# Performance work log

Measured on AMD Instinct MI355X. Metric: run time of the kernel, lower is better.

Reference implementation:

```python
import jax, jax.numpy as jnp
import numpy as np

N = 10000      # nodes
E = 160000     # edges
F_IN = 84
H = 256
P = 4          # powers [0,1,2,3]
L = 3          # mixhop layers


def setup_inputs() -> dict:
    key = jax.random.key(0)
    ks = jax.random.split(key, 10)
    s = 0.05
    inp = {}
    inp["x"] = jax.random.normal(ks[0], (N, F_IN), jnp.float32)
    inp["edge_index"] = jax.random.randint(ks[1], (2, E), 0, N, dtype=jnp.int32)
    inp["w_in"] = jax.random.normal(ks[2], (F_IN, H), jnp.float32) * s
    inp["b_in"] = jnp.zeros((H,), jnp.float32)
    inp["mh_w0"] = jax.random.normal(ks[3], (P, H, H), jnp.float32) * s
    inp["mh_b0"] = jnp.zeros((P, H), jnp.float32)
    inp["mh_w12"] = jax.random.normal(ks[4], (2, P, P * H, H), jnp.float32) * s
    inp["mh_b12"] = jnp.zeros((2, P, H), jnp.float32)
    inp["ln_g"] = jnp.ones((L, P * H), jnp.float32)
    inp["ln_b"] = jnp.zeros((L, P * H), jnp.float32)
    inp["w1"] = jax.random.normal(ks[5], (P * H, H), jnp.float32) * s
    inp["b1"] = jnp.zeros((H,), jnp.float32)
    inp["w2"] = jax.random.normal(ks[6], (H, H // 2), jnp.float32) * s
    inp["b2"] = jnp.zeros((H // 2,), jnp.float32)
    inp["w3"] = jax.random.normal(ks[7], (H // 2, 1), jnp.float32) * s
    inp["b3"] = jnp.zeros((1,), jnp.float32)
    return inp


def _gcn_norm(edge_index, n):
    # D^{-1/2} (A + I) D^{-1/2}, PyG gcn_norm with add_self_loops=True
    loop = jnp.arange(n, dtype=edge_index.dtype)
    src = jnp.concatenate([edge_index[0], loop])
    dst = jnp.concatenate([edge_index[1], loop])
    deg = jax.ops.segment_sum(jnp.ones(src.shape[0], jnp.float32), dst, num_segments=n)
    dinv = jnp.where(deg > 0, deg ** -0.5, 0.0)
    return src, dst, dinv[src] * dinv[dst]


def _propagate(h, src, dst, w, n):
    # out[i] = sum_{(j->i)} w_e * h[j]
    return jax.ops.segment_sum(h[src] * w[:, None], dst, num_segments=n)


def _mixhop(h, src, dst, w, n, W, B):
    outs = [h @ W[0] + B[0]]  # power 0
    for p in range(1, W.shape[0]):
        h = _propagate(h, src, dst, w, n)
        outs.append(h @ W[p] + B[p])
    return jnp.concatenate(outs, axis=-1)  # [n, P*H]


def _layernorm(x, g, b, eps=1e-5):
    mu = x.mean(-1, keepdims=True)
    var = x.var(-1, keepdims=True)
    return (x - mu) * jax.lax.rsqrt(var + eps) * g + b


def reference(x, edge_index, w_in, b_in, mh_w0, mh_b0, mh_w12, mh_b12,
              ln_g, ln_b, w1, b1, w2, b2, w3, b3):
    gelu = lambda t: jax.nn.gelu(t, approximate=False)  # torch default (erf)
    n = x.shape[0]
    src, dst, w = _gcn_norm(edge_index, n)
    h = gelu(x @ w_in + b_in)
    for i in range(L):
        W, B = (mh_w0, mh_b0) if i == 0 else (mh_w12[i - 1], mh_b12[i - 1])
        h = _mixhop(h, src, dst, w, n, W, B)
        h = gelu(_layernorm(h, ln_g[i], ln_b[i]))
        # dropout inactive at inference
    h = gelu(h @ w1 + b1)
    h = gelu(h @ w2 + b2)
    out = h @ w3 + b3
    return out.squeeze(-1)  # [N]
```

## Files before the change

kernel.cpp:

```cpp
#include <hip/hip_runtime.h>

typedef unsigned short u16;
typedef unsigned int u32;
typedef __bf16 bf16x8 __attribute__((ext_vector_type(8)));
typedef float f32x4 __attribute__((ext_vector_type(4)));

#define NN 10000
#define EE 160000
#define MPAD 10112

__device__ inline float b2f(u16 u) { return __uint_as_float(((u32)u) << 16); }
__device__ inline u16 f2b(float f) {
    u32 u = __float_as_uint(f);
    return (u16)((u + 0x7fffu + ((u >> 16) & 1u)) >> 16);
}
__device__ inline float gelu_f(float x) {
    return 0.5f * x * (1.0f + erff(x * 0.70710678118654752f));
}
__device__ inline void load_lds16(const u16* g, u16* l) {
    __builtin_amdgcn_global_load_lds((const __attribute__((address_space(1))) u32*)g,
                                     (__attribute__((address_space(3))) u32*)l, 16, 0, 0);
}

__global__ __launch_bounds__(256) void k_count(const int* __restrict__ dst, int* __restrict__ cnt) {
    int e = blockIdx.x * 256 + threadIdx.x;
    if (e < EE) atomicAdd(&cnt[dst[e]], 1);
}

__global__ __launch_bounds__(256) void k_scan(const int* __restrict__ cnt, int* __restrict__ rowptr,
                                              int* __restrict__ cursor, float* __restrict__ dinv) {
    __shared__ int part[256];
    const int t = threadIdx.x;
    const int CH = 40;
    int base = t * CH;
    int ssum = 0;
    for (int k = 0; k < CH; k++) { int i = base + k; if (i < NN) ssum += cnt[i]; }
    part[t] = ssum;
    __syncthreads();
    for (int off = 1; off < 256; off <<= 1) {
        int v = (t >= off) ? part[t - off] : 0;
        __syncthreads();
        part[t] += v;
        __syncthreads();
    }
    int run = part[t] - ssum;
    for (int k = 0; k < CH; k++) {
        int i = base + k;
        if (i < NN) {
            rowptr[i] = run; cursor[i] = run;
            int c = cnt[i];
            dinv[i] = rsqrtf((float)(c + 1));
            run += c;
        }
    }
    if (t == 255) rowptr[NN] = run;
}

__global__ __launch_bounds__(256) void k_fill(const int* __restrict__ src, const int* __restrict__ dst,
                                              int* __restrict__ cursor, int* __restrict__ cols,
                                              float* __restrict__ vals, const float* __restrict__ dinv) {
    int e = blockIdx.x * 256 + threadIdx.x;
    if (e < EE) {
        int s = src[e], d = dst[e];
        int pos = atomicAdd(&cursor[d], 1);
        cols[pos] = s;
        vals[pos] = dinv[s] * dinv[d];
    }
}

__global__ __launch_bounds__(256) void k_padx(const float* __restrict__ x, u16* __restrict__ xp) {
    int idx = blockIdx.x * 256 + threadIdx.x;
    if (idx >= MPAD * 128) return;
    int r = idx >> 7, c = idx & 127;
    u16 v = 0;
    if (r < NN && c < 84) v = f2b(x[(size_t)r * 84 + c]);
    xp[idx] = v;
}

struct TT { const float* src; u16* dst; int K, Nc, Kp; };
__global__ __launch_bounds__(256) void k_transT(TT t0, TT t1, TT t2, TT t3, TT t4) {
    int b = blockIdx.x; TT T;
    if (b < 8)        { T = t0; }
    else if (b < 72)  { T = t1; b -= 8; }
    else if (b < 584) { T = t2; b -= 72; }
    else if (b < 648) { T = t3; b -= 584; }
    else              { T = t4; b -= 648; }
    int tk = (T.Kp + 63) >> 6, tn = T.Nc >> 6;
    int bb  = b / (tk * tn);
    int rem = b - bb * (tk * tn);
    int k0 = (rem / tn) * 64, n0 = (rem % tn) * 64;
    __shared__ u16 tile[64][65];
    const float* src = T.src + (size_t)bb * T.K * T.Nc;
    u16* dst = T.dst + (size_t)bb * T.Nc * T.Kp;
    int c = threadIdx.x & 63, r0 = threadIdx.x >> 6;
#pragma unroll
    for (int i = 0; i < 16; i++) {
        int r = r0 + i * 4;
        int k = k0 + r;
        u16 v = 0;
        if (k < T.K) v = f2b(src[(size_t)k * T.Nc + n0 + c]);
        tile[r][c] = v;
    }
    __syncthreads();
    int rr = threadIdx.x & 63, cc0 = threadIdx.x >> 6;
#pragma unroll
    for (int i = 0; i < 16; i++) {
        int cc = cc0 + i * 4;
        int k = k0 + rr;
        if (k < T.Kp) dst[(size_t)(n0 + cc) * T.Kp + k] = tile[rr][cc];
    }
}

struct CvtSrcs { const float *b_in, *mh_b0, *mh_b12, *ln_g, *ln_b, *b1, *b2, *w3, *b3; };
__global__ __launch_bounds__(256) void k_cvt_all(CvtSrcs S, u16* __restrict__ dst) {
    int i = blockIdx.x * 256 + threadIdx.x;
    const float* s; int base;
    if (i < 256)       { s = S.b_in;   base = 0; }
    else if (i < 1280) { s = S.mh_b0;  base = 256; }
    else if (i < 3328) { s = S.mh_b12; base = 1280; }
    else if (i < 6400) { s = S.ln_g;   base = 3328; }
    else if (i < 9472) { s = S.ln_b;   base = 6400; }
    else if (i < 9728) { s = S.b1;     base = 9472; }
    else if (i < 9856) { s = S.b2;     base = 9728; }
    else if (i < 9984) { s = S.w3;     base = 9856; }
    else if (i < 9985) { s = S.b3;     base = 9984; }
    else return;
    dst[i] = f2b(s[i - base]);
}

template<int TM, int TN, int ACT, int EPI, int BATCH>
__global__ __launch_bounds__(256) void k_gemm(const u16* __restrict__ A0, const u16* __restrict__ A1,
                                              const u16* __restrict__ A2, const u16* __restrict__ A3,
                                              const u16* __restrict__ Bt, const u16* __restrict__ bias,
                                              u16* __restrict__ C, u16* __restrict__ Z,
                                              int K, int ldc, int col0, int NB_M, int NB_N) {
    constexpr int AM = TM / 32, AN = TN / 32;
    constexpr int CA = TM / 16, CB = TN / 16;
    constexpr int NCH = (CA + CB) / 4;
    constexpr int SLOT = (TM + TN) * 32;
    __shared__ __align__(16) u16 Sh[4][SLOT];
    int id = blockIdx.x;
    int g8 = id & 7, sIdx = id >> 3;
    int nb = sIdx % NB_N, jb = sIdx / NB_N;
    int mb = g8 + 8 * jb;
    if (mb >= NB_M) return;
    const u16* A = A0;
    if (BATCH) {
        int z = blockIdx.y;
        if (z == 1) A = A1; else if (z == 2) A = A2; else if (z == 3) A = A3;
        Bt   += (size_t)z * 256 * K;
        bias += z * 256;
        col0 += z * 256;
    }
    const int t = threadIdx.x;
    const int wv = t >> 6, lane = t & 63;
    const int wm = wv >> 1, wn = wv & 1;
    const int quad = lane >> 4, l16 = lane & 15;
    const int tileM = mb * TM, tileN = nb * TN;

    f32x4 acc[AM][AN] = {};

    const int rch = lane >> 2, c8 = (lane & 3) * 8;
    const u16* gsrc[NCH];
    int lofs[NCH];
#pragma unroll
    for (int i = 0; i < NCH; i++) {
        int c = wv + 4 * i;
        if (c < CA) {
            gsrc[i] = A + (size_t)(tileM + c * 16 + rch) * K + c8;
            lofs[i] = c * 512 + lane * 8;
        } else {
            int cc = c - CA;
            gsrc[i] = Bt + (size_t)(tileN + cc * 16 + rch) * K + c8;
            lofs[i] = TM * 32 + cc * 512 + lane * 8;
        }
    }

#pragma unroll
    for (int i = 0; i < NCH; i++) load_lds16(gsrc[i], &Sh[0][lofs[i]]);
#pragma unroll
    for (int i = 0; i < NCH; i++) load_lds16(gsrc[i] + 32, &Sh[1][lofs[i]]);

    const int npair = K >> 6;
    for (int p = 0; p < npair; p++) {
        __syncthreads();
        int cur = (p & 1) << 1;
        int nxt = cur ^ 2;
        int kc = p << 6;
        if (kc + 64 < K) {
#pragma unroll
            for (int i = 0; i < NCH; i++) load_lds16(gsrc[i] + kc + 64, &Sh[nxt][lofs[i]]);
#pragma unroll
            for (int i = 0; i < NCH; i++) load_lds16(gsrc[i] + kc + 96, &Sh[nxt + 1][lofs[i]]);
        }
#pragma unroll
        for (int h = 0; h < 2; h++) {
            const u16* S = Sh[cur + h];
            bf16x8 af[AM], bfr[AN];
#pragma unroll
            for (int tm = 0; tm < AM; tm++)
                af[tm] = *(const bf16x8*)&S[(wm * (TM / 2) + tm * 16 + l16) * 32 + quad * 8];
#pragma unroll
            for (int tn = 0; tn < AN; tn++)
                bfr[tn] = *(const bf16x8*)&S[TM * 32 + (wn * (TN / 2) + tn * 16 + l16) * 32 + quad * 8];
#pragma unroll
            for (int tm = 0; tm < AM; tm++)
#pragma unroll
                for (int tn = 0; tn < AN; tn++)
                    acc[tm][tn] = __builtin_amdgcn_mfma_f32_16x16x32_bf16(af[tm], bfr[tn], acc[tm][tn], 0, 0, 0);
        }
    }

#pragma unroll
    for (int tm = 0; tm < AM; tm++)
#pragma unroll
        for (int tn = 0; tn < AN; tn++)
#pragma unroll
            for (int r = 0; r < 4; r++) {
                int row = tileM + wm * (TM / 2) + tm * 16 + quad * 4 + r;
                int col = tileN + wn * (TN / 2) + tn * 16 + l16;
                float v = acc[tm][tn][r];
                if (EPI == 2) {
                    if (col < 256) C[(size_t)row * 1024 + col] = f2b(v + b2f(bias[col]));
                    else           Z[(size_t)row * 768 + (col - 256)] = f2b(v);
                } else {
                    v += b2f(bias[col]);
                    if (ACT) v = gelu_f(v);
                    C[(size_t)row * ldc + col0 + col] = f2b(v);
                }
            }
}

template<int CAT0>
__global__ __launch_bounds__(256) void k_propw(const u16* __restrict__ hin, int W, int G,
                                               const int* __restrict__ rowptr, const int* __restrict__ cols,
                                               const float* __restrict__ vals, const float* __restrict__ dinv,
                                               u16* __restrict__ concat, const u16* __restrict__ bias,
                                               int col0, u16* __restrict__ out2) {
    int unit = blockIdx.x * 4 + (threadIdx.x >> 6);
    if (unit >= NN * G) return;
    int g = unit / NN, node = unit - g * NN;
    int lane = threadIdx.x & 63;
    int half = lane >> 5, fl = lane & 31;
    const u16* base = hin + g * 256 + fl * 8;
    float a0 = 0, a1 = 0, a2 = 0, a3 = 0, a4 = 0, a5 = 0, a6 = 0, a7 = 0;
    if (half == 1) {
        float di = dinv[node], sw = di * di;
        bf16x8 sv = *(const bf16x8*)(base + (size_t)node * W);
        a0 = sw * (float)sv[0]; a1 = sw * (float)sv[1]; a2 = sw * (float)sv[2]; a3 = sw * (float)sv[3];
        a4 = sw * (float)sv[4]; a5 = sw * (float)sv[5]; a6 = sw * (float)sv[6]; a7 = sw * (float)sv[7];
    }
    int s = rowptr[node], e = rowptr[node + 1];
    int q = s + half;
    for (; q + 6 < e; q += 8) {
        int j0 = cols[q], j1 = cols[q + 2], j2 = cols[q + 4], j3 = cols[q + 6];
        float w0 = vals[q], w1 = vals[q + 2], w2 = vals[q + 4], w3 = vals[q + 6];
        bf16x8 v0 = *(const bf16x8*)(base + (size_t)j0 * W);
        bf16x8 v1 = *(const bf16x8*)(base + (size_t)j1 * W);
        bf16x8 v2 = *(const bf16x8*)(base + (size_t)j2 * W);
        bf16x8 v3 = *(const bf16x8*)(base + (size_t)j3 * W);
        a0 += w0 * (float)v0[0] + w1 * (float)v1[0] + w2 * (float)v2[0] + w3 * (float)v3[0];
        a1 += w0 * (float)v0[1] + w1 * (float)v1[1] + w2 * (float)v2[1] + w3 * (float)v3[1];
        a2 += w0 * (float)v0[2] + w1 * (float)v1[2] + w2 * (float)v2[2] + w3 * (float)v3[2];
        a3 += w0 * (float)v0[3] + w1 * (float)v1[3] + w2 * (float)v2[3] + w3 * (float)v3[3];
        a4 += w0 * (float)v0[4] + w1 * (float)v1[4] + w2 * (float)v2[4] + w3 * (float)v3[4];
        a5 += w0 * (float)v0[5] + w1 * (float)v1[5] + w2 * (float)v2[5] + w3 * (float)v3[5];
        a6 += w0 * (float)v0[6] + w1 * (float)v1[6] + w2 * (float)v2[6] + w3 * (float)v3[6];
        a7 += w0 * (float)v0[7] + w1 * (float)v1[7] + w2 * (float)v2[7] + w3 * (float)v3[7];
    }
    for (; q + 2 < e; q += 4) {
        int j0 = cols[q], j1 = cols[q + 2];
        float w0 = vals[q], w1 = vals[q + 2];
        bf16x8 v0 = *(const bf16x8*)(base + (size_t)j0 * W);
        bf16x8 v1 = *(const bf16x8*)(base + (size_t)j1 * W);
        a0 += w0 * (float)v0[0] + w1 * (float)v1[0];
        a1 += w0 * (float)v0[1] + w1 * (float)v1[1];
        a2 += w0 * (float)v0[2] + w1 * (float)v1[2];
        a3 += w0 * (float)v0[3] + w1 * (float)v1[3];
        a4 += w0 * (float)v0[4] + w1 * (float)v1[4];
        a5 += w0 * (float)v0[5] + w1 * (float)v1[5];
        a6 += w0 * (float)v0[6] + w1 * (float)v1[6];
        a7 += w0 * (float)v0[7] + w1 * (float)v1[7];
    }
    if (q < e) {
        int j = cols[q];
        float w = vals[q];
        bf16x8 v = *(const bf16x8*)(base + (size_t)j * W);
        a0 += w * (float)v[0]; a1 += w * (float)v[1]; a2 += w * (float)v[2]; a3 += w * (float)v[3];
        a4 += w * (float)v[4]; a5 += w * (float)v[5]; a6 += w * (float)v[6]; a7 += w * (float)v[7];
    }
    a0 += __shfl_down(a0, 32); a1 += __shfl_down(a1, 32);
    a2 += __shfl_down(a2, 32); a3 += __shfl_down(a3, 32);
    a4 += __shfl_down(a4, 32); a5 += __shfl_down(a5, 32);
    a6 += __shfl_down(a6, 32); a7 += __shfl_down(a7, 32);
    if (half == 0) {
        int f = fl * 8;
        union { u16 u[8]; uint4 v; } pk;
        if (CAT0 && g == 0) {
            pk.u[0] = f2b(a0 + b2f(bias[f + 0])); pk.u[1] = f2b(a1 + b2f(bias[f + 1]));
            pk.u[2] = f2b(a2 + b2f(bias[f + 2])); pk.u[3] = f2b(a3 + b2f(bias[f + 3]));
            pk.u[4] = f2b(a4 + b2f(bias[f + 4])); pk.u[5] = f2b(a5 + b2f(bias[f + 5]));
            pk.u[6] = f2b(a6 + b2f(bias[f + 6])); pk.u[7] = f2b(a7 + b2f(bias[f + 7]));
            *(uint4*)(concat + (size_t)node * 1024 + col0 + f) = pk.v;
        } else {
            int W2 = W - CAT0 * 256;
            pk.u[0] = f2b(a0); pk.u[1] = f2b(a1); pk.u[2] = f2b(a2); pk.u[3] = f2b(a3);
            pk.u[4] = f2b(a4); pk.u[5] = f2b(a5); pk.u[6] = f2b(a6); pk.u[7] = f2b(a7);
            *(uint4*)(out2 + (size_t)node * W2 + (g - CAT0) * 256 + f) = pk.v;
        }
    }
}

__global__ __launch_bounds__(256) void k_ln_gelu(const u16* __restrict__ X, const u16* __restrict__ g,
                                                 const u16* __restrict__ b, u16* __restrict__ out) {
    __shared__ float red[256];
    const int row = blockIdx.x, t = threadIdx.x;
    ushort4 xv = *(const ushort4*)(X + (size_t)row * 1024 + t * 4);
    float x0 = b2f(xv.x), x1 = b2f(xv.y), x2 = b2f(xv.z), x3 = b2f(xv.w);
    red[t] = x0 + x1 + x2 + x3;
    __syncthreads();
    for (int off = 128; off; off >>= 1) {
        if (t < off) red[t] += red[t + off];
        __syncthreads();
    }
    float mu = red[0] * (1.f / 1024.f);
    __syncthreads();
    float d0 = x0 - mu, d1 = x1 - mu, d2 = x2 - mu, d3 = x3 - mu;
    red[t] = d0 * d0 + d1 * d1 + d2 * d2 + d3 * d3;
    __syncthreads();
    for (int off = 128; off; off >>= 1) {
        if (t < off) red[t] += red[t + off];
        __syncthreads();
    }
    float rs = rsqrtf(red[0] * (1.f / 1024.f) + 1e-5f);
    int c = t * 4;
    ushort4 gv = *(const ushort4*)(g + c);
    ushort4 bv = *(const ushort4*)(b + c);
    ushort4 o;
    o.x = f2b(gelu_f(d0 * rs * b2f(gv.x) + b2f(bv.x)));
    o.y = f2b(gelu_f(d1 * rs * b2f(gv.y) + b2f(bv.y)));
    o.z = f2b(gelu_f(d2 * rs * b2f(gv.z) + b2f(bv.z)));
    o.w = f2b(gelu_f(d3 * rs * b2f(gv.w) + b2f(bv.w)));
    *(ushort4*)(out + (size_t)row * 1024 + c) = o;
}

__global__ __launch_bounds__(256) void k_final(const u16* __restrict__ h, const u16* __restrict__ w3,
                                               const u16* __restrict__ b3, float* __restrict__ out) {
    int gw = (blockIdx.x * 256 + threadIdx.x) >> 6;
    int lane = threadIdx.x & 63;
    if (gw >= NN) return;
    u32 hv = *(const u32*)(h + (size_t)gw * 128 + lane * 2);
    u32 wv = *(const u32*)(w3 + lane * 2);
    float s = b2f((u16)(hv & 0xffff)) * b2f((u16)(wv & 0xffff)) +
              b2f((u16)(hv >> 16)) * b2f((u16)(wv >> 16));
    for (int off = 32; off; off >>= 1) s += __shfl_down(s, off);
    if (lane == 0) out[gw] = s + b2f(b3[0]);
}

extern "C" void kernel_launch(void* const* d_in, const int* in_sizes, int n_in,
                              void* d_out, int out_size, void* d_ws, size_t ws_size,
                              hipStream_t stream) {
    (void)in_sizes; (void)n_in; (void)out_size; (void)ws_size;
    const float* x  = (const float*)d_in[0];
    const int*   ei = (const int*)d_in[1];
    float* out = (float*)d_out;

    char* p = (char*)d_ws;
    auto alloc = [&](size_t bytes) { char* q = p; p += (bytes + 255) & ~(size_t)255; return q; };
    int*   cnt    = (int*)alloc(NN * 4);
    int*   rowptr = (int*)alloc((NN + 1) * 4);
    int*   cursor = (int*)alloc(NN * 4);
    float* dinv   = (float*)alloc(NN * 4);
    int*   cols   = (int*)alloc(EE * 4);
    float* vals   = (float*)alloc(EE * 4);
    u16*   xp     = (u16*)alloc((size_t)MPAD * 128 * 2);
    u16*   wbuf   = (u16*)alloc((size_t)2686976 * 2);
    u16*   smallC = (u16*)alloc(10240 * 2);
    u16*   S1     = (u16*)alloc((size_t)MPAD * 256 * 2);
    u16*   S2     = (u16*)alloc((size_t)MPAD * 256 * 2);
    u16*   S3     = (u16*)alloc((size_t)MPAD * 256 * 2);
    u16*   S4     = (u16*)alloc((size_t)MPAD * 256 * 2);
    u16*   Zb     = (u16*)alloc((size_t)MPAD * 768 * 2);
    u16*   Y2     = (u16*)alloc((size_t)MPAD * 512 * 2);
    u16*   Y3     = (u16*)alloc((size_t)MPAD * 256 * 2);
    u16*   bufA   = (u16*)alloc((size_t)MPAD * 1024 * 2);
    u16*   concat = (u16*)alloc((size_t)MPAD * 1024 * 2);

    u16* winT  = wbuf;
    u16* w0T   = wbuf + 32768;
    u16* w12T  = wbuf + 294912;
    u16* w1T   = wbuf + 2392064;
    u16* w2T   = wbuf + 2654208;
    u16* binC  = smallC;
    u16* mb0C  = smallC + 256;
    u16* mb12C = smallC + 1280;
    u16* lngC  = smallC + 3328;
    u16* lnbC  = smallC + 6400;
    u16* b1C   = smallC + 9472;
    u16* b2C   = smallC + 9728;
    u16* w3C   = smallC + 9856;
    u16* b3C   = smallC + 9984;

    const int* srcA = ei;
    const int* dstA = ei + EE;

    hipMemsetAsync(cnt, 0, NN * 4, stream);

    k_padx<<<(MPAD * 128 + 255) / 256, 256, 0, stream>>>(x, xp);
    TT t0{(const float*)d_in[2],  winT, 84,   256, 128};
    TT t1{(const float*)d_in[4],  w0T,  256,  256, 256};
    TT t2{(const float*)d_in[6],  w12T, 1024, 256, 1024};
    TT t3{(const float*)d_in[10], w1T,  1024, 256, 1024};
    TT t4{(const float*)d_in[12], w2T,  256,  128, 256};
    k_transT<<<656, 256, 0, stream>>>(t0, t1, t2, t3, t4);
    CvtSrcs CS{(const float*)d_in[3], (const float*)d_in[5], (const float*)d_in[7],
               (const float*)d_in[8], (const float*)d_in[9], (const float*)d_in[11],
               (const float*)d_in[13], (const float*)d_in[14], (const float*)d_in[15]};
    k_cvt_all<<<40, 256, 0, stream>>>(CS, smallC);

    k_count<<<(EE + 255) / 256, 256, 0, stream>>>(dstA, cnt);
    k_scan<<<1, 256, 0, stream>>>(cnt, rowptr, cursor, dinv);
    k_fill<<<(EE + 255) / 256, 256, 0, stream>>>(srcA, dstA, cursor, cols, vals, dinv);

    auto gx = [](int nbm, int nbn) { return 8 * ((nbm + 7) / 8) * nbn; };

    k_gemm<128, 64, 1, 0, 0><<<gx(79, 4), 256, 0, stream>>>(xp, xp, xp, xp, winT, binC, S1, nullptr, 128, 256, 0, 79, 4);

    k_propw<0><<<2500, 256, 0, stream>>>(S1, 256, 1, rowptr, cols, vals, dinv, nullptr, nullptr, 0, S2);
    k_propw<0><<<2500, 256, 0, stream>>>(S2, 256, 1, rowptr, cols, vals, dinv, nullptr, nullptr, 0, S3);
    k_propw<0><<<2500, 256, 0, stream>>>(S3, 256, 1, rowptr, cols, vals, dinv, nullptr, nullptr, 0, S4);
    k_gemm<128, 64, 0, 0, 1><<<dim3(gx(79, 4), 4), 256, 0, stream>>>(S1, S2, S3, S4, w0T, mb0C, concat, nullptr, 256, 1024, 0, 79, 4);
    k_ln_gelu<<<NN, 256, 0, stream>>>(concat, lngC, lnbC, bufA);

    for (int L = 0; L < 2; L++) {
        const u16* WT = w12T + (size_t)L * 1024 * 1024;
        const u16* BB = mb12C + L * 1024;
        k_gemm<128, 64, 0, 2, 0><<<gx(79, 16), 256, 0, stream>>>(bufA, bufA, bufA, bufA, WT, BB, concat, Zb, 1024, 0, 0, 79, 16);
        k_propw<1><<<7500, 256, 0, stream>>>(Zb, 768, 3, rowptr, cols, vals, dinv, concat, BB + 256, 256, Y2);
        k_propw<1><<<5000, 256, 0, stream>>>(Y2, 512, 2, rowptr, cols, vals, dinv, concat, BB + 512, 512, Y3);
        k_propw<1><<<2500, 256, 0, stream>>>(Y3, 256, 1, rowptr, cols, vals, dinv, concat, BB + 768, 768, Y3);
        k_ln_gelu<<<NN, 256, 0, stream>>>(concat, lngC + (L + 1) * 1024, lnbC + (L + 1) * 1024, bufA);
    }

    k_gemm<64, 64, 1, 0, 0><<<gx(158, 4), 256, 0, stream>>>(bufA, bufA, bufA, bufA, w1T, b1C, S1, nullptr, 1024, 256, 0, 158, 4);
    k_gemm<64, 64, 1, 0, 0><<<gx(158, 2), 256, 0, stream>>>(S1, S1, S1, S1, w2T, b2C, S2, nullptr, 256, 128, 0, 158, 2);
    k_final<<<2500, 256, 0, stream>>>(S2, w3C, b3C, out);
}
```

Measured before the change: 479.9 us.

## Store propagation input in fp8, fuse ingest kernels and final projection into GEMM

Stores the intermediate Z buffer (768 columns fed into graph propagation) as fp8 instead of bf16, halving gather bytes in the largest propagation kernel. It also deepens the edge unroll to 8 gathers in flight, merges the padding, transpose, bias-convert and degree-count kernels into one launch, and fuses the w3 dot product into the w2 GEMM epilogue. The fp8 storage lowers precision of the propagated features and could affect accuracy.

```diff
diff --git a/kernel.cpp b/kernel.cpp
--- a/kernel.cpp
+++ b/kernel.cpp
@@ -1,9 +1,11 @@
 #include <hip/hip_runtime.h>
 
 typedef unsigned short u16;
+typedef unsigned char u8;
 typedef unsigned int u32;
 typedef __bf16 bf16x8 __attribute__((ext_vector_type(8)));
 typedef float f32x4 __attribute__((ext_vector_type(4)));
+typedef float f32x2 __attribute__((ext_vector_type(2)));
 
 #define NN 10000
 #define EE 160000
@@ -14,17 +16,15 @@
     u32 u = __float_as_uint(f);
     return (u16)((u + 0x7fffu + ((u >> 16) & 1u)) >> 16);
 }
+__device__ inline u8 f2f8(float v) {
+    return (u8)(__builtin_amdgcn_cvt_pk_fp8_f32(v, v, 0, false) & 0xff);
+}
 __device__ inline float gelu_f(float x) {
     return 0.5f * x * (1.0f + erff(x * 0.70710678118654752f));
 }
 __device__ inline void load_lds16(const u16* g, u16* l) {
     __builtin_amdgcn_global_load_lds((const __attribute__((address_space(1))) u32*)g,
                                      (__attribute__((address_space(3))) u32*)l, 16, 0, 0);
-}
-
-__global__ __launch_bounds__(256) void k_count(const int* __restrict__ dst, int* __restrict__ cnt) {
-    int e = blockIdx.x * 256 + threadIdx.x;
-    if (e < EE) atomicAdd(&cnt[dst[e]], 1);
 }
 
 __global__ __launch_bounds__(256) void k_scan(const int* __restrict__ cnt, int* __restrict__ rowptr,
@@ -68,77 +68,85 @@
     }
 }
 
-__global__ __launch_bounds__(256) void k_padx(const float* __restrict__ x, u16* __restrict__ xp) {
-    int idx = blockIdx.x * 256 + threadIdx.x;
-    if (idx >= MPAD * 128) return;
-    int r = idx >> 7, c = idx & 127;
-    u16 v = 0;
-    if (r < NN && c < 84) v = f2b(x[(size_t)r * 84 + c]);
-    xp[idx] = v;
-}
-
 struct TT { const float* src; u16* dst; int K, Nc, Kp; };
-__global__ __launch_bounds__(256) void k_transT(TT t0, TT t1, TT t2, TT t3, TT t4) {
-    int b = blockIdx.x; TT T;
-    if (b < 8)        { T = t0; }
-    else if (b < 72)  { T = t1; b -= 8; }
-    else if (b < 584) { T = t2; b -= 72; }
-    else if (b < 648) { T = t3; b -= 584; }
-    else              { T = t4; b -= 648; }
-    int tk = (T.Kp + 63) >> 6, tn = T.Nc >> 6;
-    int bb  = b / (tk * tn);
-    int rem = b - bb * (tk * tn);
-    int k0 = (rem / tn) * 64, n0 = (rem % tn) * 64;
-    __shared__ u16 tile[64][65];
-    const float* src = T.src + (size_t)bb * T.K * T.Nc;
-    u16* dst = T.dst + (size_t)bb * T.Nc * T.Kp;
-    int c = threadIdx.x & 63, r0 = threadIdx.x >> 6;
-#pragma unroll
-    for (int i = 0; i < 16; i++) {
-        int r = r0 + i * 4;
-        int k = k0 + r;
+struct CvtSrcs { const float *b_in, *mh_b0, *mh_b12, *ln_g, *ln_b, *b1, *b2, *w3, *b3; };
+__global__ __launch_bounds__(256) void k_ingest(TT t0, TT t1, TT t2, TT t3, TT t4,
+                                                const float* __restrict__ x, u16* __restrict__ xp,
+                                                CvtSrcs S, u16* __restrict__ smallC,
+                                                const int* __restrict__ dstA, int* __restrict__ cnt) {
+    int b = blockIdx.x;
+    const int t = threadIdx.x;
+    if (b < 656) {
+        TT T;
+        if (b < 8)        { T = t0; }
+        else if (b < 72)  { T = t1; b -= 8; }
+        else if (b < 584) { T = t2; b -= 72; }
+        else if (b < 648) { T = t3; b -= 584; }
+        else              { T = t4; b -= 648; }
+        int tk = (T.Kp + 63) >> 6, tn = T.Nc >> 6;
+        int bb  = b / (tk * tn);
+        int rem = b - bb * (tk * tn);
+        int k0 = (rem / tn) * 64, n0 = (rem % tn) * 64;
+        __shared__ u16 tile[64][65];
+        const float* src = T.src + (size_t)bb * T.K * T.Nc;
+        u16* dst = T.dst + (size_t)bb * T.Nc * T.Kp;
+        int c = t & 63, r0 = t >> 6;
+#pragma unroll
+        for (int i = 0; i < 16; i++) {
+            int r = r0 + i * 4;
+            int k = k0 + r;
+            u16 v = 0;
+            if (k < T.K) v = f2b(src[(size_t)k * T.Nc + n0 + c]);
+            tile[r][c] = v;
+        }
+        __syncthreads();
+        int rr = t & 63, cc0 = t >> 6;
+#pragma unroll
+        for (int i = 0; i < 16; i++) {
+            int cc = cc0 + i * 4;
+            int k = k0 + rr;
+            if (k < T.Kp) dst[(size_t)(n0 + cc) * T.Kp + k] = tile[rr][cc];
+        }
+    } else if (b < 5712) {
+        int idx = (b - 656) * 256 + t;
+        int r = idx >> 7, c = idx & 127;
         u16 v = 0;
-        if (k < T.K) v = f2b(src[(size_t)k * T.Nc + n0 + c]);
-        tile[r][c] = v;
-    }
-    __syncthreads();
-    int rr = threadIdx.x & 63, cc0 = threadIdx.x >> 6;
-#pragma unroll
-    for (int i = 0; i < 16; i++) {
-        int cc = cc0 + i * 4;
-        int k = k0 + rr;
-        if (k < T.Kp) dst[(size_t)(n0 + cc) * T.Kp + k] = tile[rr][cc];
-    }
-}
-
-struct CvtSrcs { const float *b_in, *mh_b0, *mh_b12, *ln_g, *ln_b, *b1, *b2, *w3, *b3; };
-__global__ __launch_bounds__(256) void k_cvt_all(CvtSrcs S, u16* __restrict__ dst) {
-    int i = blockIdx.x * 256 + threadIdx.x;
-    const float* s; int base;
-    if (i < 256)       { s = S.b_in;   base = 0; }
-    else if (i < 1280) { s = S.mh_b0;  base = 256; }
-    else if (i < 3328) { s = S.mh_b12; base = 1280; }
-    else if (i < 6400) { s = S.ln_g;   base = 3328; }
-    else if (i < 9472) { s = S.ln_b;   base = 6400; }
-    else if (i < 9728) { s = S.b1;     base = 9472; }
-    else if (i < 9856) { s = S.b2;     base = 9728; }
-    else if (i < 9984) { s = S.w3;     base = 9856; }
-    else if (i < 9985) { s = S.b3;     base = 9984; }
-    else return;
-    dst[i] = f2b(s[i - base]);
+        if (r < NN && c < 84) v = f2b(x[(size_t)r * 84 + c]);
+        xp[idx] = v;
+    } else if (b < 5752) {
+        int i = (b - 5712) * 256 + t;
+        const float* s; int base;
+        if (i < 256)       { s = S.b_in;   base = 0; }
+        else if (i < 1280) { s = S.mh_b0;  base = 256; }
+        else if (i < 3328) { s = S.mh_b12; base = 1280; }
+        else if (i < 6400) { s = S.ln_g;   base = 3328; }
+        else if (i < 9472) { s = S.ln_b;   base = 6400; }
+        else if (i < 9728) { s = S.b1;     base = 9472; }
+        else if (i < 9856) { s = S.b2;     base = 9728; }
+        else if (i < 9984) { s = S.w3;     base = 9856; }
+        else if (i < 9985) { s = S.b3;     base = 9984; }
+        else return;
+        smallC[i] = f2b(s[i - base]);
+    } else {
+        int e = (b - 5752) * 256 + t;
+        if (e < EE) atomicAdd(&cnt[dstA[e]], 1);
+    }
 }
 
 template<int TM, int TN, int ACT, int EPI, int BATCH>
 __global__ __launch_bounds__(256) void k_gemm(const u16* __restrict__ A0, const u16* __restrict__ A1,
                                               const u16* __restrict__ A2, const u16* __restrict__ A3,
                                               const u16* __restrict__ Bt, const u16* __restrict__ bias,
-                                              u16* __restrict__ C, u16* __restrict__ Z,
+                                              u16* __restrict__ C, u8* __restrict__ Z,
+                                              const u16* __restrict__ w3c, const u16* __restrict__ b3c,
+                                              float* __restrict__ fout,
                                               int K, int ldc, int col0, int NB_M, int NB_N) {
     constexpr int AM = TM / 32, AN = TN / 32;
     constexpr int CA = TM / 16, CB = TN / 16;
     constexpr int NCH = (CA + CB) / 4;
     constexpr int SLOT = (TM + TN) * 32;
     __shared__ __align__(16) u16 Sh[4][SLOT];
+    __shared__ float shred[2][64];
     int id = blockIdx.x;
     int g8 = id & 7, sIdx = id >> 3;
     int nb = sIdx % NB_N, jb = sIdx / NB_N;
@@ -195,20 +203,43 @@
         }
 #pragma unroll
         for (int h = 0; h < 2; h++) {
-            const u16* S = Sh[cur + h];
+            const u16* Sb = Sh[cur + h];
             bf16x8 af[AM], bfr[AN];
 #pragma unroll
             for (int tm = 0; tm < AM; tm++)
-                af[tm] = *(const bf16x8*)&S[(wm * (TM / 2) + tm * 16 + l16) * 32 + quad * 8];
+                af[tm] = *(const bf16x8*)&Sb[(wm * (TM / 2) + tm * 16 + l16) * 32 + quad * 8];
 #pragma unroll
             for (int tn = 0; tn < AN; tn++)
-                bfr[tn] = *(const bf16x8*)&S[TM * 32 + (wn * (TN / 2) + tn * 16 + l16) * 32 + quad * 8];
+                bfr[tn] = *(const bf16x8*)&Sb[TM * 32 + (wn * (TN / 2) + tn * 16 + l16) * 32 + quad * 8];
 #pragma unroll
             for (int tm = 0; tm < AM; tm++)
 #pragma unroll
                 for (int tn = 0; tn < AN; tn++)
                     acc[tm][tn] = __builtin_amdgcn_mfma_f32_16x16x32_bf16(af[tm], bfr[tn], acc[tm][tn], 0, 0, 0);
         }
+    }
+
+    if (EPI == 3) {
+#pragma unroll
+        for (int tm = 0; tm < AM; tm++)
+#pragma unroll
+            for (int r = 0; r < 4; r++) {
+                float psum = 0.f;
+#pragma unroll
+                for (int tn = 0; tn < AN; tn++) {
+                    int col = wn * (TN / 2) + tn * 16 + l16;
+                    float v = gelu_f(acc[tm][tn][r] + b2f(bias[col]));
+                    psum += v * b2f(w3c[col]);
+                }
+                for (int off = 8; off; off >>= 1) psum += __shfl_down(psum, off);
+                if (l16 == 0) shred[wn][wm * (TM / 2) + tm * 16 + quad * 4 + r] = psum;
+            }
+        __syncthreads();
+        if (t < TM) {
+            int row = tileM + t;
+            if (row < NN) fout[row] = shred[0][t] + shred[1][t] + b2f(b3c[0]);
+        }
+        return;
     }
 
 #pragma unroll
@@ -222,7 +253,7 @@
                 float v = acc[tm][tn][r];
                 if (EPI == 2) {
                     if (col < 256) C[(size_t)row * 1024 + col] = f2b(v + b2f(bias[col]));
-                    else           Z[(size_t)row * 768 + (col - 256)] = f2b(v);
+                    else           Z[(size_t)row * 768 + (col - 256)] = f2f8(v);
                 } else {
                     v += b2f(bias[col]);
                     if (ACT) v = gelu_f(v);
@@ -231,82 +262,88 @@
             }
 }
 
-template<int CAT0>
-__global__ __launch_bounds__(256) void k_propw(const u16* __restrict__ hin, int W, int G,
-                                               const int* __restrict__ rowptr, const int* __restrict__ cols,
-                                               const float* __restrict__ vals, const float* __restrict__ dinv,
-                                               u16* __restrict__ concat, const u16* __restrict__ bias,
-                                               int col0, u16* __restrict__ out2) {
+__device__ inline void f8acc(uint2 u, float w, float* a) {
+    f32x2 p0 = __builtin_amdgcn_cvt_pk_f32_fp8(u.x, false);
+    f32x2 p1 = __builtin_amdgcn_cvt_pk_f32_fp8(u.x, true);
+    f32x2 p2 = __builtin_amdgcn_cvt_pk_f32_fp8(u.y, false);
+    f32x2 p3 = __builtin_amdgcn_cvt_pk_f32_fp8(u.y, true);
+    a[0] += w * p0.x; a[1] += w * p0.y; a[2] += w * p1.x; a[3] += w * p1.y;
+    a[4] += w * p2.x; a[5] += w * p2.y; a[6] += w * p3.x; a[7] += w * p3.y;
+}
+__device__ inline void bfacc(bf16x8 v, float w, float* a) {
+#pragma unroll
+    for (int i = 0; i < 8; i++) a[i] += w * (float)v[i];
+}
+template<int IN8>
+__global__ __launch_bounds__(256) void k_prop(const void* __restrict__ hinv, int W, int G, int OW,
+                                              const int* __restrict__ rowptr, const int* __restrict__ cols,
+                                              const float* __restrict__ vals, const float* __restrict__ dinv,
+                                              u16* __restrict__ concat, const u16* __restrict__ bias,
+                                              int col0, u16* __restrict__ out2) {
     int unit = blockIdx.x * 4 + (threadIdx.x >> 6);
     if (unit >= NN * G) return;
     int g = unit / NN, node = unit - g * NN;
     int lane = threadIdx.x & 63;
     int half = lane >> 5, fl = lane & 31;
-    const u16* base = hin + g * 256 + fl * 8;
-    float a0 = 0, a1 = 0, a2 = 0, a3 = 0, a4 = 0, a5 = 0, a6 = 0, a7 = 0;
+    const u8* base8 = (const u8*)hinv + g * 256 + fl * 8;
+    const u16* baseb = (const u16*)hinv + g * 256 + fl * 8;
+    float a[8] = {0, 0, 0, 0, 0, 0, 0, 0};
     if (half == 1) {
-        float di = dinv[node], sw = di * di;
-        bf16x8 sv = *(const bf16x8*)(base + (size_t)node * W);
-        a0 = sw * (float)sv[0]; a1 = sw * (float)sv[1]; a2 = sw * (float)sv[2]; a3 = sw * (float)sv[3];
-        a4 = sw * (float)sv[4]; a5 = sw * (float)sv[5]; a6 = sw * (float)sv[6]; a7 = sw * (float)sv[7];
+        float sw = dinv[node] * dinv[node];
+        if (IN8) f8acc(*(const uint2*)(base8 + (size_t)node * W), sw, a);
+        else     bfacc(*(const bf16x8*)(baseb + (size_t)node * W), sw, a);
     }
     int s = rowptr[node], e = rowptr[node + 1];
     int q = s + half;
-    for (; q + 6 < e; q += 8) {
-        int j0 = cols[q], j1 = cols[q + 2], j2 = cols[q + 4], j3 = cols[q + 6];
-        float w0 = vals[q], w1 = vals[q + 2], w2 = vals[q + 4], w3 = vals[q + 6];
-        bf16x8 v0 = *(const bf16x8*)(base + (size_t)j0 * W);
-        bf16x8 v1 = *(const bf16x8*)(base + (size_t)j1 * W);
-        bf16x8 v2 = *(const bf16x8*)(base + (size_t)j2 * W);
-        bf16x8 v3 = *(const bf16x8*)(base + (size_t)j3 * W);
-        a0 += w0 * (float)v0[0] + w1 * (float)v1[0] + w2 * (float)v2[0] + w3 * (float)v3[0];
-        a1 += w0 * (float)v0[1] + w1 * (float)v1[1] + w2 * (float)v2[1] + w3 * (float)v3[1];
-        a2 += w0 * (float)v0[2] + w1 * (float)v1[2] + w2 * (float)v2[2] + w3 * (float)v3[2];
-        a3 += w0 * (float)v0[3] + w1 * (float)v1[3] + w2 * (float)v2[3] + w3 * (float)v3[3];
-        a4 += w0 * (float)v0[4] + w1 * (float)v1[4] + w2 * (float)v2[4] + w3 * (float)v3[4];
-        a5 += w0 * (float)v0[5] + w1 * (float)v1[5] + w2 * (float)v2[5] + w3 * (float)v3[5];
-        a6 += w0 * (float)v0[6] + w1 * (float)v1[6] + w2 * (float)v2[6] + w3 * (float)v3[6];
-        a7 += w0 * (float)v0[7] + w1 * (float)v1[7] + w2 * (float)v2[7] + w3 * (float)v3[7];
+    for (; q + 14 < e; q += 16) {
+        int j[8]; float w[8];
+#pragma unroll
+        for (int i = 0; i < 8; i++) { j[i] = cols[q + 2 * i]; w[i] = vals[q + 2 * i]; }
+        if (IN8) {
+            uint2 v[8];
+#pragma unroll
+            for (int i = 0; i < 8; i++) v[i] = *(const uint2*)(base8 + (size_t)j[i] * W);
+#pragma unroll
+            for (int i = 0; i < 8; i++) f8acc(v[i], w[i], a);
+        } else {
+            bf16x8 v[8];
+#pragma unroll
+            for (int i = 0; i < 8; i++) v[i] = *(const bf16x8*)(baseb + (size_t)j[i] * W);
+#pragma unroll
+            for (int i = 0; i < 8; i++) bfacc(v[i], w[i], a);
+        }
     }
     for (; q + 2 < e; q += 4) {
         int j0 = cols[q], j1 = cols[q + 2];
         float w0 = vals[q], w1 = vals[q + 2];
-        bf16x8 v0 = *(const bf16x8*)(base + (size_t)j0 * W);
-        bf16x8 v1 = *(const bf16x8*)(base + (size_t)j1 * W);
-        a0 += w0 * (float)v0[0] + w1 * (float)v1[0];
-        a1 += w0 * (float)v0[1] + w1 * (float)v1[1];
-        a2 += w0 * (float)v0[2] + w1 * (float)v1[2];
-        a3 += w0 * (float)v0[3] + w1 * (float)v1[3];
-        a4 += w0 * (float)v0[4] + w1 * (float)v1[4];
-        a5 += w0 * (float)v0[5] + w1 * (float)v1[5];
-        a6 += w0 * (float)v0[6] + w1 * (float)v1[6];
-        a7 += w0 * (float)v0[7] + w1 * (float)v1[7];
+        if (IN8) {
+            uint2 v0 = *(const uint2*)(base8 + (size_t)j0 * W);
+            uint2 v1 = *(const uint2*)(base8 + (size_t)j1 * W);
+            f8acc(v0, w0, a); f8acc(v1, w1, a);
+        } else {
+            bf16x8 v0 = *(const bf16x8*)(baseb + (size_t)j0 * W);
+            bf16x8 v1 = *(const bf16x8*)(baseb + (size_t)j1 * W);
+            bfacc(v0, w0, a); bfacc(v1, w1, a);
+        }
     }
     if (q < e) {
-        int j = cols[q];
-        float w = vals[q];
-        bf16x8 v = *(const bf16x8*)(base + (size_t)j * W);
-        a0 += w * (float)v[0]; a1 += w * (float)v[1]; a2 += w * (float)v[2]; a3 += w * (float)v[3];
-        a4 += w * (float)v[4]; a5 += w * (float)v[5]; a6 += w * (float)v[6]; a7 += w * (float)v[7];
-    }
-    a0 += __shfl_down(a0, 32); a1 += __shfl_down(a1, 32);
-    a2 += __shfl_down(a2, 32); a3 += __shfl_down(a3, 32);
-    a4 += __shfl_down(a4, 32); a5 += __shfl_down(a5, 32);
-    a6 += __shfl_down(a6, 32); a7 += __shfl_down(a7, 32);
+        if (IN8) f8acc(*(const uint2*)(base8 + (size_t)cols[q] * W), vals[q], a);
+        else     bfacc(*(const bf16x8*)(baseb + (size_t)cols[q] * W), vals[q], a);
+    }
+#pragma unroll
+    for (int i = 0; i < 8; i++) a[i] += __shfl_down(a[i], 32);
     if (half == 0) {
         int f = fl * 8;
         union { u16 u[8]; uint4 v; } pk;
-        if (CAT0 && g == 0) {
-            pk.u[0] = f2b(a0 + b2f(bias[f + 0])); pk.u[1] = f2b(a1 + b2f(bias[f + 1]));
-            pk.u[2] = f2b(a2 + b2f(bias[f + 2])); pk.u[3] = f2b(a3 + b2f(bias[f + 3]));
-            pk.u[4] = f2b(a4 + b2f(bias[f + 4])); pk.u[5] = f2b(a5 + b2f(bias[f + 5]));
-            pk.u[6] = f2b(a6 + b2f(bias[f + 6])); pk.u[7] = f2b(a7 + b2f(bias[f + 7]));
+        if (bias && g == 0) {
+#pragma unroll
+            for (int i = 0; i < 8; i++) pk.u[i] = f2b(a[i] + b2f(bias[f + i]));
             *(uint4*)(concat + (size_t)node * 1024 + col0 + f) = pk.v;
         } else {
-            int W2 = W - CAT0 * 256;
-            pk.u[0] = f2b(a0); pk.u[1] = f2b(a1); pk.u[2] = f2b(a2); pk.u[3] = f2b(a3);
-            pk.u[4] = f2b(a4); pk.u[5] = f2b(a5); pk.u[6] = f2b(a6); pk.u[7] = f2b(a7);
-            *(uint4*)(out2 + (size_t)node * W2 + (g - CAT0) * 256 + f) = pk.v;
+#pragma unroll
+            for (int i = 0; i < 8; i++) pk.u[i] = f2b(a[i]);
+            int gg = g - (bias ? 1 : 0);
+            *(uint4*)(out2 + (size_t)node * OW + gg * 256 + f) = pk.v;
         }
     }
 }
@@ -342,19 +379,6 @@
     o.z = f2b(gelu_f(d2 * rs * b2f(gv.z) + b2f(bv.z)));
     o.w = f2b(gelu_f(d3 * rs * b2f(gv.w) + b2f(bv.w)));
     *(ushort4*)(out + (size_t)row * 1024 + c) = o;
-}
-
-__global__ __launch_bounds__(256) void k_final(const u16* __restrict__ h, const u16* __restrict__ w3,
-                                               const u16* __restrict__ b3, float* __restrict__ out) {
-    int gw = (blockIdx.x * 256 + threadIdx.x) >> 6;
-    int lane = threadIdx.x & 63;
-    if (gw >= NN) return;
-    u32 hv = *(const u32*)(h + (size_t)gw * 128 + lane * 2);
-    u32 wv = *(const u32*)(w3 + lane * 2);
-    float s = b2f((u16)(hv & 0xffff)) * b2f((u16)(wv & 0xffff)) +
-              b2f((u16)(hv >> 16)) * b2f((u16)(wv >> 16));
-    for (int off = 32; off; off >>= 1) s += __shfl_down(s, off);
-    if (lane == 0) out[gw] = s + b2f(b3[0]);
 }
 
 extern "C" void kernel_launch(void* const* d_in, const int* in_sizes, int n_in,
@@ -380,7 +404,7 @@
     u16*   S2     = (u16*)alloc((size_t)MPAD * 256 * 2);
     u16*   S3     = (u16*)alloc((size_t)MPAD * 256 * 2);
     u16*   S4     = (u16*)alloc((size_t)MPAD * 256 * 2);
-    u16*   Zb     = (u16*)alloc((size_t)MPAD * 768 * 2);
+    u8*    Zb     = (u8*)alloc((size_t)MPAD * 768);
     u16*   Y2     = (u16*)alloc((size_t)MPAD * 512 * 2);
     u16*   Y3     = (u16*)alloc((size_t)MPAD * 256 * 2);
     u16*   bufA   = (u16*)alloc((size_t)MPAD * 1024 * 2);
@@ -406,43 +430,44 @@
 
     hipMemsetAsync(cnt, 0, NN * 4, stream);
 
-    k_padx<<<(MPAD * 128 + 255) / 256, 256, 0, stream>>>(x, xp);
     TT t0{(const float*)d_in[2],  winT, 84,   256, 128};
     TT t1{(const float*)d_in[4],  w0T,  256,  256, 256};
     TT t2{(const float*)d_in[6],  w12T, 1024, 256, 1024};
     TT t3{(const float*)d_in[10], w1T,  1024, 256, 1024};
     TT t4{(const float*)d_in[12], w2T,  256,  128, 256};
-    k_transT<<<656, 256, 0, stream>>>(t0, t1, t2, t3, t4);
     CvtSrcs CS{(const float*)d_in[3], (const float*)d_in[5], (const float*)d_in[7],
                (const float*)d_in[8], (const float*)d_in[9], (const float*)d_in[11],
                (const float*)d_in[13], (const float*)d_in[14], (const float*)d_in[15]};
-    k_cvt_all<<<40, 256, 0, stream>>>(CS, smallC);
-
-    k_count<<<(EE + 255) / 256, 256, 0, stream>>>(dstA, cnt);
+    k_ingest<<<6377, 256, 0, stream>>>(t0, t1, t2, t3, t4, x, xp, CS, smallC, dstA, cnt);
+
     k_scan<<<1, 256, 0, stream>>>(cnt, rowptr, cursor, dinv);
     k_fill<<<(EE + 255) / 256, 256, 0, stream>>>(srcA, dstA, cursor, cols, vals, dinv);
 
     auto gx = [](int nbm, int nbn) { return 8 * ((nbm + 7) / 8) * nbn; };
 
-    k_gemm<128, 64, 1, 0, 0><<<gx(79, 4), 256, 0, stream>>>(xp, xp, xp, xp, winT, binC, S1, nullptr, 128, 256, 0, 79, 4);
-
-    k_propw<0><<<2500, 256, 0, stream>>>(S1, 256, 1, rowptr, cols, vals, dinv, nullptr, nullptr, 0, S2);
-    k_propw<0><<<2500, 256, 0, stream>>>(S2, 256, 1, rowptr, cols, vals, dinv, nullptr, nullptr, 0, S3);
-    k_propw<0><<<2500, 256, 0, stream>>>(S3, 256, 1, rowptr, cols, vals, dinv, nullptr, nullptr, 0, S4);
-    k_gemm<128, 64, 0, 0, 1><<<dim3(gx(79, 4), 4), 256, 0, stream>>>(S1, S2, S3, S4, w0T, mb0C, concat, nullptr, 256, 1024, 0, 79, 4);
+    k_gemm<128, 64, 1, 0, 0><<<gx(79, 4), 256, 0, stream>>>(xp, xp, xp, xp, winT, binC, S1, nullptr,
+                                                            nullptr, nullptr, nullptr, 128, 256, 0, 79, 4);
+
+    k_prop<0><<<2500, 256, 0, stream>>>(S1, 256, 1, 256, rowptr, cols, vals, dinv, nullptr, nullptr, 0, S2);
+    k_prop<0><<<2500, 256, 0, stream>>>(S2, 256, 1, 256, rowptr, cols, vals, dinv, nullptr, nullptr, 0, S3);
+    k_prop<0><<<2500, 256, 0, stream>>>(S3, 256, 1, 256, rowptr, cols, vals, dinv, nullptr, nullptr, 0, S4);
+    k_gemm<128, 64, 0, 0, 1><<<dim3(gx(79, 4), 4), 256, 0, stream>>>(S1, S2, S3, S4, w0T, mb0C, concat, nullptr,
+                                                                     nullptr, nullptr, nullptr, 256, 1024, 0, 79, 4);
     k_ln_gelu<<<NN, 256, 0, stream>>>(concat, lngC, lnbC, bufA);
 
     for (int L = 0; L < 2; L++) {
         const u16* WT = w12T + (size_t)L * 1024 * 1024;
         const u16* BB = mb12C + L * 1024;
-        k_gemm<128, 64, 0, 2, 0><<<gx(79, 16), 256, 0, stream>>>(bufA, bufA, bufA, bufA, WT, BB, concat, Zb, 1024, 0, 0, 79, 16);
-        k_propw<1><<<7500, 256, 0, stream>>>(Zb, 768, 3, rowptr, cols, vals, dinv, concat, BB + 256, 256, Y2);
-        k_propw<1><<<5000, 256, 0, stream>>>(Y2, 512, 2, rowptr, cols, vals, dinv, concat, BB + 512, 512, Y3);
-        k_propw<1><<<2500, 256, 0, stream>>>(Y3, 256, 1, rowptr, cols, vals, dinv, concat, BB + 768, 768, Y3);
+        k_gemm<128, 64, 0, 2, 0><<<gx(79, 16), 256, 0, stream>>>(bufA, bufA, bufA, bufA, WT, BB, concat, Zb,
+                                                                 nullptr, nullptr, nullptr, 1024, 0, 0, 79, 16);
+        k_prop<1><<<7500, 256, 0, stream>>>(Zb, 768, 3, 512, rowptr, cols, vals, dinv, concat, BB + 256, 256, Y2);
+        k_prop<0><<<5000, 256, 0, stream>>>(Y2, 512, 2, 256, rowptr, cols, vals, dinv, concat, BB + 512, 512, Y3);
+        k_prop<0><<<2500, 256, 0, stream>>>(Y3, 256, 1, 0, rowptr, cols, vals, dinv, concat, BB + 768, 768, nullptr);
         k_ln_gelu<<<NN, 256, 0, stream>>>(concat, lngC + (L + 1) * 1024, lnbC + (L + 1) * 1024, bufA);
     }
 
-    k_gemm<64, 64, 1, 0, 0><<<gx(158, 4), 256, 0, stream>>>(bufA, bufA, bufA, bufA, w1T, b1C, S1, nullptr, 1024, 256, 0, 158, 4);
-    k_gemm<64, 64, 1, 0, 0><<<gx(158, 2), 256, 0, stream>>>(S1, S1, S1, S1, w2T, b2C, S2, nullptr, 256, 128, 0, 158, 2);
-    k_final<<<2500, 256, 0, stream>>>(S2, w3C, b3C, out);
-}
+    k_gemm<64, 64, 1, 0, 0><<<gx(158, 4), 256, 0, stream>>>(bufA, bufA, bufA, bufA, w1T, b1C, S1, nullptr,
+                                                            nullptr, nullptr, nullptr, 1024, 256, 0, 158, 4);
+    k_gemm<64, 128, 0, 3, 0><<<gx(158, 1), 256, 0, stream>>>(S1, S1, S1, S1, w2T, b2C, nullptr, nullptr,
+                                                             w3C, b3C, out, 256, 0, 0, 158, 1);
+}
```

Result: no change. 482.8 us (+0.6%).
